# Optimization experiments

Hardware: AMD Instinct MI355X
Metric: run time of the kernel (lower is better)

## Reference

```python
import jax, jax.numpy as jnp
import numpy as np

WS = 11      # window_size
SIGMA = 1.5
CH = 4       # channels / groups (hardcoded in forward)
SCALE = 1.0


def _gaussian_window(dtype):
    x = np.arange(WS, dtype=np.float64) - WS // 2
    g = np.exp(-(x ** 2) / (2.0 * SIGMA ** 2))
    g = g / g.sum()
    w2 = np.outer(g, g).astype(np.float32)          # [WS, WS]
    w = np.broadcast_to(w2, (CH, 1, WS, WS)).copy()  # [O, I/groups, kH, kW]
    return jnp.asarray(w, dtype=dtype)


def _dwconv(x, w):
    # depthwise conv2d, groups=CH, VALID padding (matches F.conv2d default padding=0)
    return jax.lax.conv_general_dilated(
        x, w, window_strides=(1, 1), padding='VALID',
        dimension_numbers=('NCHW', 'OIHW', 'NCHW'),
        feature_group_count=CH)


def setup_inputs() -> dict:
    key = jax.random.key(0)
    k1, k2 = jax.random.split(key)
    X = jax.random.normal(k1, (16, 4, 512, 512), dtype=jnp.float32)
    Y = jax.random.normal(k2, (16, 4, 512, 512), dtype=jnp.float32)
    return {"X": X, "Y": Y}


def reference(X, Y):
    w = _gaussian_window(X.dtype)
    muX = _dwconv(X, w)
    muY = _dwconv(Y, w)
    muX_sq, muY_sq, muXY = muX * muX, muY * muY, muX * muY
    sigmaX_sq = _dwconv(X * X, w) - muX_sq
    sigmaY_sq = _dwconv(Y * Y, w) - muY_sq
    sigmaXY = _dwconv(X * Y, w) - muXY
    C1 = (0.01 * SCALE) ** 2
    C2 = (0.03 * SCALE) ** 2
    v1 = 2.0 * sigmaXY + C2
    v2 = sigmaX_sq + sigmaY_sq + C2
    ssim_map = (2.0 * muXY + C1) * v1 / ((muX_sq + muY_sq + C1) * v2)
    return 1.0 - ssim_map.mean()
```

## Files before the change

kernel.cpp:

```cpp
#include <hip/hip_runtime.h>
#include <hip/hip_bf16.h>
#include <cmath>


#define IMG   512
#define ODIM  502
#define SC    16
#define BR    128
#define WPB   4
#define BC    (SC * WPB)
#define GX    8
#define GY    4
#define NC    64
#define NBLK  (GX * GY * NC)
#define NVT   8

typedef float          f32x4  __attribute__((ext_vector_type(4)));
typedef __bf16         bf16x8 __attribute__((ext_vector_type(8)));
typedef __bf16         bf16x4 __attribute__((ext_vector_type(4)));
typedef short          s16x4  __attribute__((ext_vector_type(4)));
typedef unsigned int   u32x2  __attribute__((ext_vector_type(2)));
typedef unsigned int   u32x4  __attribute__((ext_vector_type(4)));

union F8 { bf16x8 v; __bf16 b[8]; u32x4 q; };
union F4 { bf16x4 v; s16x4 s; __bf16 b[4]; u32x2 q; };

__device__ __forceinline__ unsigned short bfbits(float f) {
    __bf16 h = (__bf16)f;
    return __builtin_bit_cast(unsigned short, h);
}

__device__ __forceinline__ f32x4 mfma16(const F4& a, const F4& b, f32x4 c) {
    return __builtin_amdgcn_mfma_f32_16x16x16bf16_1k(a.s, b.s, c, 0, 0, 0);
}

struct GaussW { float g[11]; };

__global__ __launch_bounds__(256, 5) void ssim_mfma_kernel(
    const float* __restrict__ X, const float* __restrict__ Y,
    float* __restrict__ partial, GaussW gw)
{
    __shared__ unsigned short wl[16][40];
    __shared__ float wsum[WPB];

    const int tid  = threadIdx.x;
    const int lane = tid & 63;
    const int wave = tid >> 6;
    const int m    = lane & 15;
    const int g    = lane >> 4;

    for (int t = tid; t < 16 * 40; t += 256) {
        const int mm = t / 40, kk = t - 40 * mm;
        const int d  = kk - mm;
        wl[mm][kk] = bfbits((kk < 32 && d >= 0 && d < 11) ? gw.g[d] : 0.f);
    }
    __syncthreads();

    const int gx0 = blockIdx.x * BC + SC * wave;
    const int gy0 = blockIdx.y * BR;
    const int nc  = blockIdx.z;
    const float* __restrict__ Xp = X + (size_t)nc * IMG * IMG;
    const float* __restrict__ Yp = Y + (size_t)nc * IMG * IMG;

    F8 wf;  wf.q  = *(const u32x4*)&wl[m][8 * g];
    F4 wa0; wa0.q = *(const u32x2*)&wl[m][4 * g];
    F4 wa1; wa1.q = *(const u32x2*)&wl[m][16 + 4 * g];
    const f32x4 z = {0.f, 0.f, 0.f, 0.f};

    const int cs = min(gx0 + 8 * g, IMG - 8);

    auto computeH = [&](F4 (&hd)[5], int rt) {
        const int gy = min(gy0 + 16 * rt + m, IMG - 1);
        const float* xr = Xp + gy * IMG + cs;
        const float* yr = Yp + gy * IMG + cs;
        const f32x4 a0 = *(const f32x4*)xr;
        const f32x4 a1 = *(const f32x4*)(xr + 4);
        const f32x4 b0 = *(const f32x4*)yr;
        const f32x4 b1 = *(const f32x4*)(yr + 4);

        F8 fx, fy, fxx, fyy, fxy;
#pragma unroll
        for (int j = 0; j < 4; ++j) {
            fx.b[j]      = (__bf16)a0[j];
            fx.b[4 + j]  = (__bf16)a1[j];
            fy.b[j]      = (__bf16)b0[j];
            fy.b[4 + j]  = (__bf16)b1[j];
            fxx.b[j]     = (__bf16)(a0[j] * a0[j]);
            fxx.b[4 + j] = (__bf16)(a1[j] * a1[j]);
            fyy.b[j]     = (__bf16)(b0[j] * b0[j]);
            fyy.b[4 + j] = (__bf16)(b1[j] * b1[j]);
            fxy.b[j]     = (__bf16)(a0[j] * b0[j]);
            fxy.b[4 + j] = (__bf16)(a1[j] * b1[j]);
        }
        const f32x4 dX  = __builtin_amdgcn_mfma_f32_16x16x32_bf16(fx.v,  wf.v, z, 0, 0, 0);
        const f32x4 dY  = __builtin_amdgcn_mfma_f32_16x16x32_bf16(fy.v,  wf.v, z, 0, 0, 0);
        const f32x4 dXX = __builtin_amdgcn_mfma_f32_16x16x32_bf16(fxx.v, wf.v, z, 0, 0, 0);
        const f32x4 dYY = __builtin_amdgcn_mfma_f32_16x16x32_bf16(fyy.v, wf.v, z, 0, 0, 0);
        const f32x4 dXY = __builtin_amdgcn_mfma_f32_16x16x32_bf16(fxy.v, wf.v, z, 0, 0, 0);
#pragma unroll
        for (int i = 0; i < 4; ++i) {
            hd[0].b[i] = (__bf16)dX[i];
            hd[1].b[i] = (__bf16)dY[i];
            hd[2].b[i] = (__bf16)dXX[i];
            hd[3].b[i] = (__bf16)dYY[i];
            hd[4].b[i] = (__bf16)dXY[i];
        }
    };

    F4 hh[2][5];
    computeH(hh[0], 0);

    float acc = 0.f;
#pragma unroll
    for (int vt = 0; vt < NVT; ++vt) {
        computeH(hh[(vt + 1) & 1], vt + 1);
        const F4 (&h0)[5] = hh[vt & 1];
        const F4 (&h1)[5] = hh[(vt + 1) & 1];

        f32x4 e[5];
#pragma unroll
        for (int q = 0; q < 5; ++q) {
            e[q] = mfma16(wa1, h1[q], z);
            e[q] = mfma16(wa0, h0[q], e[q]);
        }
        const float C1 = 1e-4f, C2 = 9e-4f;
#pragma unroll
        for (int i = 0; i < 4; ++i) {
            const int gy = gy0 + 16 * vt + 4 * g + i;
            const int gx = gx0 + m;
            const float mX = e[0][i], mY = e[1][i];
            const float muXX = mX * mX;
            const float muYY = mY * mY;
            const float muXY = mX * mY;
            const float sXX = e[2][i] - muXX;
            const float sYY = e[3][i] - muYY;
            const float sXY = e[4][i] - muXY;
            const float num = (2.f * muXY + C1) * (2.f * sXY + C2);
            const float den = (muXX + muYY + C1) * (sXX + sYY + C2);
            const float val = __fdividef(num, den);
            if (gy < ODIM && gx < ODIM) acc += val;
        }
    }

#pragma unroll
    for (int off = 32; off > 0; off >>= 1)
        acc += __shfl_down(acc, off, 64);

    if (lane == 0) wsum[wave] = acc;
    __syncthreads();
    if (tid == 0) {
        const float tsum = (wsum[0] + wsum[1]) + (wsum[2] + wsum[3]);
        partial[((size_t)blockIdx.z * gridDim.y + blockIdx.y) * gridDim.x + blockIdx.x] = tsum;
    }
}

__global__ __launch_bounds__(512) void ssim_finish_kernel(
    const float* __restrict__ partial, float* __restrict__ out)
{
    __shared__ double sd[512];
    const float4* p4 = (const float4*)partial;
    const float4 v = p4[threadIdx.x];
    double local = ((double)v.x + (double)v.y) + ((double)v.z + (double)v.w);
    sd[threadIdx.x] = local;
    __syncthreads();
    for (int s = 256; s > 0; s >>= 1) {
        if (threadIdx.x < s) sd[threadIdx.x] += sd[threadIdx.x + s];
        __syncthreads();
    }
    if (threadIdx.x == 0) {
        const double cnt = (double)NC * (double)ODIM * (double)ODIM;
        out[0] = (float)(1.0 - sd[0] / cnt);
    }
}

extern "C" void kernel_launch(void* const* d_in, const int* in_sizes, int n_in,
                              void* d_out, int out_size, void* d_ws, size_t ws_size,
                              hipStream_t stream) {
    const float* X = (const float*)d_in[0];
    const float* Y = (const float*)d_in[1];
    float* out = (float*)d_out;
    float* partial = (float*)d_ws;

    GaussW gw;
    {
        double gd[11], s = 0.0;
        for (int i = 0; i < 11; ++i) {
            const double x = (double)(i - 5);
            gd[i] = std::exp(-(x * x) / (2.0 * 1.5 * 1.5));
            s += gd[i];
        }
        for (int i = 0; i < 11; ++i) gw.g[i] = (float)(gd[i] / s);
    }

    dim3 grid(GX, GY, NC);
    ssim_mfma_kernel<<<grid, 256, 0, stream>>>(X, Y, partial, gw);
    ssim_finish_kernel<<<1, 512, 0, stream>>>(partial, out);
}
```

Before: 48.16 us.

## Fuse final reduction via atomic last-block, prefetch raw rows, pack bf16 conversions

The separate finish kernel is replaced by a last-block-done pattern: each block writes its partial sum, fences, bumps an atomic counter, and the last block reduces all partials. Global loads are split from the MFMA work and issued two row-tiles ahead to hide memory latency. Element-wise bf16 writes are replaced by packed 32-bit conversions. The change also relaxes the occupancy hint and adds a memset launch for the counter, which may offset the launch saved by dropping the finish kernel.

After: 116.4 us. 2.42x slower.

```diff
diff --git a/kernel.cpp b/kernel.cpp
--- a/kernel.cpp
+++ b/kernel.cpp
@@ -14,6 +14,7 @@
 #define NC    64
 #define NBLK  (GX * GY * NC)
 #define NVT   8
+#define NHT   9
 
 typedef float          f32x4  __attribute__((ext_vector_type(4)));
 typedef __bf16         bf16x8 __attribute__((ext_vector_type(8)));
@@ -22,26 +23,33 @@
 typedef unsigned int   u32x2  __attribute__((ext_vector_type(2)));
 typedef unsigned int   u32x4  __attribute__((ext_vector_type(4)));
 
-union F8 { bf16x8 v; __bf16 b[8]; u32x4 q; };
-union F4 { bf16x4 v; s16x4 s; __bf16 b[4]; u32x2 q; };
+union F8 { bf16x8 v; u32x4 q; };
+union F4 { bf16x4 v; s16x4 s; u32x2 q; };
 
 __device__ __forceinline__ unsigned short bfbits(float f) {
     __bf16 h = (__bf16)f;
     return __builtin_bit_cast(unsigned short, h);
 }
+__device__ __forceinline__ unsigned pk2(float lo, float hi) {
+    return ((unsigned)bfbits(hi) << 16) | (unsigned)bfbits(lo);
+}
 
 __device__ __forceinline__ f32x4 mfma16(const F4& a, const F4& b, f32x4 c) {
     return __builtin_amdgcn_mfma_f32_16x16x16bf16_1k(a.s, b.s, c, 0, 0, 0);
 }
 
 struct GaussW { float g[11]; };
-
-__global__ __launch_bounds__(256, 5) void ssim_mfma_kernel(
+struct Raw { f32x4 a0, a1, b0, b1; };
+
+__global__ __launch_bounds__(256, 4) void ssim_mfma_kernel(
     const float* __restrict__ X, const float* __restrict__ Y,
-    float* __restrict__ partial, GaussW gw)
+    float* __restrict__ partial, unsigned* __restrict__ counter,
+    float* __restrict__ out, GaussW gw)
 {
     __shared__ unsigned short wl[16][40];
     __shared__ float wsum[WPB];
+    __shared__ double sd[256];
+    __shared__ int lastFlag;
 
     const int tid  = threadIdx.x;
     const int lane = tid & 63;
@@ -69,51 +77,55 @@
 
     const int cs = min(gx0 + 8 * g, IMG - 8);
 
-    auto computeH = [&](F4 (&hd)[5], int rt) {
+    auto loadRaw = [&](Raw& r, int rt) {
         const int gy = min(gy0 + 16 * rt + m, IMG - 1);
         const float* xr = Xp + gy * IMG + cs;
         const float* yr = Yp + gy * IMG + cs;
-        const f32x4 a0 = *(const f32x4*)xr;
-        const f32x4 a1 = *(const f32x4*)(xr + 4);
-        const f32x4 b0 = *(const f32x4*)yr;
-        const f32x4 b1 = *(const f32x4*)(yr + 4);
-
+        r.a0 = *(const f32x4*)xr;  r.a1 = *(const f32x4*)(xr + 4);
+        r.b0 = *(const f32x4*)yr;  r.b1 = *(const f32x4*)(yr + 4);
+    };
+
+    auto mfmaH = [&](F4 (&hd)[5], const Raw& r) {
         F8 fx, fy, fxx, fyy, fxy;
-#pragma unroll
-        for (int j = 0; j < 4; ++j) {
-            fx.b[j]      = (__bf16)a0[j];
-            fx.b[4 + j]  = (__bf16)a1[j];
-            fy.b[j]      = (__bf16)b0[j];
-            fy.b[4 + j]  = (__bf16)b1[j];
-            fxx.b[j]     = (__bf16)(a0[j] * a0[j]);
-            fxx.b[4 + j] = (__bf16)(a1[j] * a1[j]);
-            fyy.b[j]     = (__bf16)(b0[j] * b0[j]);
-            fyy.b[4 + j] = (__bf16)(b1[j] * b1[j]);
-            fxy.b[j]     = (__bf16)(a0[j] * b0[j]);
-            fxy.b[4 + j] = (__bf16)(a1[j] * b1[j]);
-        }
+        fx.q  = u32x4{pk2(r.a0[0], r.a0[1]), pk2(r.a0[2], r.a0[3]),
+                      pk2(r.a1[0], r.a1[1]), pk2(r.a1[2], r.a1[3])};
+        fy.q  = u32x4{pk2(r.b0[0], r.b0[1]), pk2(r.b0[2], r.b0[3]),
+                      pk2(r.b1[0], r.b1[1]), pk2(r.b1[2], r.b1[3])};
+        fxx.q = u32x4{pk2(r.a0[0]*r.a0[0], r.a0[1]*r.a0[1]),
+                      pk2(r.a0[2]*r.a0[2], r.a0[3]*r.a0[3]),
+                      pk2(r.a1[0]*r.a1[0], r.a1[1]*r.a1[1]),
+                      pk2(r.a1[2]*r.a1[2], r.a1[3]*r.a1[3])};
+        fyy.q = u32x4{pk2(r.b0[0]*r.b0[0], r.b0[1]*r.b0[1]),
+                      pk2(r.b0[2]*r.b0[2], r.b0[3]*r.b0[3]),
+                      pk2(r.b1[0]*r.b1[0], r.b1[1]*r.b1[1]),
+                      pk2(r.b1[2]*r.b1[2], r.b1[3]*r.b1[3])};
+        fxy.q = u32x4{pk2(r.a0[0]*r.b0[0], r.a0[1]*r.b0[1]),
+                      pk2(r.a0[2]*r.b0[2], r.a0[3]*r.b0[3]),
+                      pk2(r.a1[0]*r.b1[0], r.a1[1]*r.b1[1]),
+                      pk2(r.a1[2]*r.b1[2], r.a1[3]*r.b1[3])};
         const f32x4 dX  = __builtin_amdgcn_mfma_f32_16x16x32_bf16(fx.v,  wf.v, z, 0, 0, 0);
         const f32x4 dY  = __builtin_amdgcn_mfma_f32_16x16x32_bf16(fy.v,  wf.v, z, 0, 0, 0);
         const f32x4 dXX = __builtin_amdgcn_mfma_f32_16x16x32_bf16(fxx.v, wf.v, z, 0, 0, 0);
         const f32x4 dYY = __builtin_amdgcn_mfma_f32_16x16x32_bf16(fyy.v, wf.v, z, 0, 0, 0);
         const f32x4 dXY = __builtin_amdgcn_mfma_f32_16x16x32_bf16(fxy.v, wf.v, z, 0, 0, 0);
-#pragma unroll
-        for (int i = 0; i < 4; ++i) {
-            hd[0].b[i] = (__bf16)dX[i];
-            hd[1].b[i] = (__bf16)dY[i];
-            hd[2].b[i] = (__bf16)dXX[i];
-            hd[3].b[i] = (__bf16)dYY[i];
-            hd[4].b[i] = (__bf16)dXY[i];
-        }
+        hd[0].q = u32x2{pk2(dX[0],  dX[1]),  pk2(dX[2],  dX[3])};
+        hd[1].q = u32x2{pk2(dY[0],  dY[1]),  pk2(dY[2],  dY[3])};
+        hd[2].q = u32x2{pk2(dXX[0], dXX[1]), pk2(dXX[2], dXX[3])};
+        hd[3].q = u32x2{pk2(dYY[0], dYY[1]), pk2(dYY[2], dYY[3])};
+        hd[4].q = u32x2{pk2(dXY[0], dXY[1]), pk2(dXY[2], dXY[3])};
     };
 
-    F4 hh[2][5];
-    computeH(hh[0], 0);
+    Raw raw[2];
+    F4  hh[2][5];
+    loadRaw(raw[0], 0);
+    loadRaw(raw[1], 1);
+    mfmaH(hh[0], raw[0]);
 
     float acc = 0.f;
 #pragma unroll
     for (int vt = 0; vt < NVT; ++vt) {
-        computeH(hh[(vt + 1) & 1], vt + 1);
+        if (vt + 2 < NHT) loadRaw(raw[vt & 1], vt + 2);
+        mfmaH(hh[(vt + 1) & 1], raw[(vt + 1) & 1]);
         const F4 (&h0)[5] = hh[vt & 1];
         const F4 (&h1)[5] = hh[(vt + 1) & 1];
 
@@ -148,28 +160,33 @@
 
     if (lane == 0) wsum[wave] = acc;
     __syncthreads();
+    const int bid = ((int)blockIdx.z * gridDim.y + blockIdx.y) * gridDim.x + blockIdx.x;
     if (tid == 0) {
         const float tsum = (wsum[0] + wsum[1]) + (wsum[2] + wsum[3]);
-        partial[((size_t)blockIdx.z * gridDim.y + blockIdx.y) * gridDim.x + blockIdx.x] = tsum;
-    }
-}
-
-__global__ __launch_bounds__(512) void ssim_finish_kernel(
-    const float* __restrict__ partial, float* __restrict__ out)
-{
-    __shared__ double sd[512];
-    const float4* p4 = (const float4*)partial;
-    const float4 v = p4[threadIdx.x];
-    double local = ((double)v.x + (double)v.y) + ((double)v.z + (double)v.w);
-    sd[threadIdx.x] = local;
+        partial[bid] = tsum;
+        __threadfence();
+        const unsigned prev = atomicAdd(counter, 1u);
+        lastFlag = (prev == NBLK - 1) ? 1 : 0;
+    }
     __syncthreads();
-    for (int s = 256; s > 0; s >>= 1) {
-        if (threadIdx.x < s) sd[threadIdx.x] += sd[threadIdx.x + s];
+
+    if (lastFlag) {
+        __threadfence();
+        const volatile float* vp = (const volatile float*)partial;
+        double local = 0.0;
+#pragma unroll
+        for (int i = 0; i < NBLK / 256; ++i)
+            local += (double)vp[tid * (NBLK / 256) + i];
+        sd[tid] = local;
         __syncthreads();
-    }
-    if (threadIdx.x == 0) {
-        const double cnt = (double)NC * (double)ODIM * (double)ODIM;
-        out[0] = (float)(1.0 - sd[0] / cnt);
+        for (int s = 128; s > 0; s >>= 1) {
+            if (tid < s) sd[tid] += sd[tid + s];
+            __syncthreads();
+        }
+        if (tid == 0) {
+            const double cnt = (double)NC * (double)ODIM * (double)ODIM;
+            out[0] = (float)(1.0 - sd[0] / cnt);
+        }
     }
 }
 
@@ -180,6 +197,9 @@
     const float* Y = (const float*)d_in[1];
     float* out = (float*)d_out;
     float* partial = (float*)d_ws;
+    unsigned* counter = (unsigned*)((char*)d_ws + NBLK * sizeof(float));
+
+    (void)hipMemsetAsync(counter, 0, sizeof(unsigned), stream);
 
     GaussW gw;
     {
@@ -193,6 +213,5 @@
     }
 
     dim3 grid(GX, GY, NC);
-    ssim_mfma_kernel<<<grid, 256, 0, stream>>>(X, Y, partial, gw);
-    ssim_finish_kernel<<<1, 512, 0, stream>>>(partial, out);
-}
+    ssim_mfma_kernel<<<grid, 256, 0, stream>>>(X, Y, partial, counter, out, gw);
+}
```
